# Kernel optimization log

Measured on AMD Instinct MI355X. Metric: run time of the kernel, lower is better.

The kernel has to match this reference:

```python
import jax, jax.numpy as jnp
import numpy as np

B, L, D, H, NL, F = 64, 197, 768, 12, 12, 3072
HD = D // H
EPS = 1e-6


def setup_inputs() -> dict:
    key = jax.random.key(0)
    ks = jax.random.split(key, 8)
    s = 0.02  # init std, matches nn.Parameter normal_(std=0.02) / xavier-ish scale
    def n(k, shape, scale=s):
        return jax.random.normal(k, shape, jnp.float32) * scale
    return {
        "x": jax.random.normal(ks[0], (B, L, D), jnp.float32),
        "pos_emb": n(ks[1], (1, L, D)),
        "ln1_g": jnp.ones((NL, D), jnp.float32),
        "ln1_b": jnp.zeros((NL, D), jnp.float32),
        "Wq": n(ks[2], (NL, D, D)), "bq": jnp.zeros((NL, D), jnp.float32),
        "Wk": n(ks[3], (NL, D, D)), "bk": jnp.zeros((NL, D), jnp.float32),
        "Wv": n(ks[4], (NL, D, D)), "bv": jnp.zeros((NL, D), jnp.float32),
        "Wo": n(ks[5], (NL, D, D)), "bo": jnp.zeros((NL, D), jnp.float32),
        "ln2_g": jnp.ones((NL, D), jnp.float32),
        "ln2_b": jnp.zeros((NL, D), jnp.float32),
        "W1": n(ks[6], (NL, D, F)), "b1": jnp.zeros((NL, F), jnp.float32),
        "W2": n(ks[7], (NL, F, D)), "b2": jnp.zeros((NL, D), jnp.float32),
        "lnf_g": jnp.ones((D,), jnp.float32),
        "lnf_b": jnp.zeros((D,), jnp.float32),
    }


def _ln(x, g, b):
    m = jnp.mean(x, axis=-1, keepdims=True)
    v = jnp.var(x, axis=-1, keepdims=True)
    return (x - m) * jax.lax.rsqrt(v + EPS) * g + b


def reference(x, pos_emb, ln1_g, ln1_b, Wq, bq, Wk, bk, Wv, bv, Wo, bo,
              ln2_g, ln2_b, W1, b1, W2, b2, lnf_g, lnf_b):
    Bv, Lv, Dv = x.shape
    nh = H
    hd = Dv // nh
    scale = 1.0 / np.sqrt(hd).astype(np.float32)

    def block(h, p):
        g1, be1, wq, bq_, wk, bk_, wv, bv_, wo, bo_, g2, be2, w1, bb1, w2, bb2 = p
        y = _ln(h, g1, be1)
        q = (y @ wq + bq_).reshape(Bv, Lv, nh, hd)
        k = (y @ wk + bk_).reshape(Bv, Lv, nh, hd)
        v = (y @ wv + bv_).reshape(Bv, Lv, nh, hd)
        scores = jnp.einsum('bqhd,bkhd->bhqk', q, k) * scale  # [B,H,L,L]
        a = jax.nn.softmax(scores, axis=-1)
        o = jnp.einsum('bhqk,bkhd->bqhd', a, v).reshape(Bv, Lv, Dv)
        h = h + (o @ wo + bo_)
        y = _ln(h, g2, be2)
        y = jax.nn.gelu(y @ w1 + bb1, approximate=False)
        y = y @ w2 + bb2
        return h + y, None

    params = (ln1_g, ln1_b, Wq, bq, Wk, bk, Wv, bv, Wo, bo,
              ln2_g, ln2_b, W1, b1, W2, b2)
    h = x + pos_emb
    h, _ = jax.lax.scan(block, h, params)
    return _ln(h, lnf_g, lnf_b)
```

## Files before the change

kernel.cpp:

```cpp
#include <hip/hip_runtime.h>
#include <hip/hip_bf16.h>
#include <cmath>

#define B_ 64
#define L_ 197
#define D_ 768
#define H_ 12
#define NL_ 12
#define F_ 3072
#define M_ (B_*L_)
#define MPAD_ 12672

typedef __bf16 bf16_t;
typedef __bf16 bf16x8 __attribute__((ext_vector_type(8)));
typedef __bf16 bf16x4 __attribute__((ext_vector_type(4)));
typedef float  f32x4  __attribute__((ext_vector_type(4)));

#define GPTR(p) ((const __attribute__((address_space(1))) void*)(p))
#define LPTR(p) ((__attribute__((address_space(3))) void*)(p))

__device__ __forceinline__ float gelu_f(float x) {
    return 0.5f * x * (1.f + erff(x * 0.70710678118654752440f));
}

__global__ __launch_bounds__(256) void k_addpos(const float4* __restrict__ x,
                                                const float4* __restrict__ pos,
                                                bf16x4* __restrict__ h,
                                                int n4, int ld4) {
    int i = blockIdx.x * 256 + threadIdx.x;
    if (i < n4) {
        float4 a = x[i];
        float4 p = pos[i % ld4];
        bf16x4 o;
        o[0] = (bf16_t)(a.x + p.x); o[1] = (bf16_t)(a.y + p.y);
        o[2] = (bf16_t)(a.z + p.z); o[3] = (bf16_t)(a.w + p.w);
        h[i] = o;
    }
}

__global__ __launch_bounds__(256) void k_prep(
        const float* __restrict__ Wq, const float* __restrict__ Wk,
        const float* __restrict__ Wv, const float* __restrict__ Wo,
        const float* __restrict__ W1, const float* __restrict__ W2,
        const float* __restrict__ bq, const float* __restrict__ bk,
        const float* __restrict__ bv,
        bf16_t* __restrict__ wqkvT, bf16_t* __restrict__ woT,
        bf16_t* __restrict__ w1T, bf16_t* __restrict__ w2T,
        float* __restrict__ bqkv) {
    int bidx = blockIdx.x;
    if (bidx < 3) {
        int i = bidx * 256 + threadIdx.x;
        if (i < D_) { bqkv[i] = bq[i]; bqkv[D_ + i] = bk[i]; bqkv[2*D_ + i] = bv[i]; }
        return;
    }
    int t = bidx - 3;
    const float* W; bf16_t* BT; int K, N;
    if (t < 576) {
        int seg = t / 144; t -= seg * 144;
        K = D_; N = D_;
        W  = (seg == 0 ? Wq : seg == 1 ? Wk : seg == 2 ? Wv : Wo);
        BT = (seg == 3 ? woT : wqkvT + (size_t)seg * 768 * D_);
    } else if (t < 1152) { t -= 576;  W = W1; BT = w1T; K = D_; N = F_; }
    else                 { t -= 1152; W = W2; BT = w2T; K = F_; N = D_; }
    const int kt = K / 64;
    const int k0 = (t % kt) * 64, n0 = (t / kt) * 64;

    __shared__ bf16_t s[64][67];
    int tid = threadIdx.x;
    int kr = tid >> 4, nc = (tid & 15) * 4;
    #pragma unroll
    for (int i = 0; i < 4; ++i) {
        float4 v = *(const float4*)(W + (size_t)(k0 + kr + i*16) * N + n0 + nc);
        s[kr + i*16][nc]     = (bf16_t)v.x;
        s[kr + i*16][nc + 1] = (bf16_t)v.y;
        s[kr + i*16][nc + 2] = (bf16_t)v.z;
        s[kr + i*16][nc + 3] = (bf16_t)v.w;
    }
    __syncthreads();
    int nr = tid >> 3, kc = (tid & 7) * 8;
    #pragma unroll
    for (int i = 0; i < 2; ++i) {
        bf16x8 o;
        #pragma unroll
        for (int j = 0; j < 8; ++j) o[j] = s[kc + j][nr + i*32];
        *(bf16x8*)(BT + (size_t)(n0 + nr + i*32) * K + k0 + kc) = o;
    }
}

template<bool BF16OUT>
__global__ __launch_bounds__(256) void k_ln(const bf16_t* __restrict__ x,
                                            const float* __restrict__ g,
                                            const float* __restrict__ bsh,
                                            void* __restrict__ out) {
    int wid = threadIdx.x >> 6, lane = threadIdx.x & 63;
    size_t row = (size_t)blockIdx.x * 4 + wid;
    const bf16x4* xr = (const bf16x4*)(x + row * D_);
    float vv[12];
    float s = 0.f, sq = 0.f;
    #pragma unroll
    for (int i = 0; i < 3; ++i) {
        bf16x4 v4 = xr[i*64 + lane];
        #pragma unroll
        for (int j = 0; j < 4; ++j) {
            float f = (float)v4[j];
            vv[i*4 + j] = f; s += f; sq += f*f;
        }
    }
    #pragma unroll
    for (int o = 1; o < 64; o <<= 1) { s += __shfl_xor(s, o); sq += __shfl_xor(sq, o); }
    float mean = s * (1.f/768.f);
    float var  = sq * (1.f/768.f) - mean*mean;
    float rstd = rsqrtf(var + 1e-6f);
    const float4* g4 = (const float4*)g;
    const float4* b4 = (const float4*)bsh;
    #pragma unroll
    for (int i = 0; i < 3; ++i) {
        float4 gg = g4[i*64 + lane], bb = b4[i*64 + lane];
        float r0 = (vv[i*4+0] - mean)*rstd*gg.x + bb.x;
        float r1 = (vv[i*4+1] - mean)*rstd*gg.y + bb.y;
        float r2 = (vv[i*4+2] - mean)*rstd*gg.z + bb.z;
        float r3 = (vv[i*4+3] - mean)*rstd*gg.w + bb.w;
        if (BF16OUT) {
            bf16x4 o4; o4[0]=(bf16_t)r0; o4[1]=(bf16_t)r1; o4[2]=(bf16_t)r2; o4[3]=(bf16_t)r3;
            ((bf16x4*)((bf16_t*)out + row * D_))[i*64 + lane] = o4;
        } else {
            float4 r; r.x=r0; r.y=r1; r.z=r2; r.w=r3;
            ((float4*)out)[row * (D_/4) + i*64 + lane] = r;
        }
    }
}

template<int EPI>
__global__ __launch_bounds__(256, 4) void k_gemm_bt(
        const bf16_t* __restrict__ A, const bf16_t* __restrict__ BT,
        const float* __restrict__ bias, const bf16_t* __restrict__ resid,
        void* __restrict__ Cout, int K, int N, int NB) {
    __shared__ bf16_t LDS_[2][128 * 64];
    bf16_t* As = LDS_[0];
    bf16_t* Bs = LDS_[1];

    const int tid = threadIdx.x, lane = tid & 63, wid = tid >> 6;
    const int g = lane >> 4, fr = lane & 15;
    const int wm = (wid >> 1) * 64, wn = (wid & 1) * 64;

    int nwg = (int)gridDim.x, orig = (int)blockIdx.x;
    int qq = nwg >> 3, rr = nwg & 7;
    int xcd = orig & 7, idx = orig >> 3;
    int wg = (xcd < rr ? xcd * (qq + 1) : rr * (qq + 1) + (xcd - rr) * qq) + idx;
    int bx = wg / NB, by = wg - bx * NB;
    const int gm0 = bx * 128, gn0 = by * 128;

    const int srl = lane >> 3;
    const int sc = ((lane & 7) ^ srl) * 8;

    f32x4 acc[4][4];
    #pragma unroll
    for (int i = 0; i < 4; ++i)
        #pragma unroll
        for (int j = 0; j < 4; ++j) acc[i][j] = (f32x4){0.f, 0.f, 0.f, 0.f};

    const bf16_t* a_src = A  + (size_t)(gm0 + wid * 32 + srl) * K + sc;
    const bf16_t* b_src = BT + (size_t)(gn0 + wid * 32 + srl) * K + sc;

    const int NT = K >> 6;
    for (int t = 0; t < NT; ++t) {
        const int k0 = t * 64;
        __syncthreads();
        #pragma unroll
        for (int i = 0; i < 4; ++i) {
            __builtin_amdgcn_global_load_lds(GPTR(a_src + (size_t)(i * 8) * K + k0),
                                             LPTR(&As[(wid * 32 + i * 8) * 64]), 16, 0, 0);
            __builtin_amdgcn_global_load_lds(GPTR(b_src + (size_t)(i * 8) * K + k0),
                                             LPTR(&Bs[(wid * 32 + i * 8) * 64]), 16, 0, 0);
        }
        __syncthreads();

        bf16x8 af[4][2], bf[4][2];
        #pragma unroll
        for (int mi = 0; mi < 4; ++mi) {
            const int row = wm + mi * 16 + fr;
            #pragma unroll
            for (int kc = 0; kc < 2; ++kc)
                af[mi][kc] = *(const bf16x8*)&As[row * 64 + (((kc * 4 + g) ^ (row & 7)) * 8)];
        }
        #pragma unroll
        for (int ni = 0; ni < 4; ++ni) {
            const int row = wn + ni * 16 + fr;
            #pragma unroll
            for (int kc = 0; kc < 2; ++kc)
                bf[ni][kc] = *(const bf16x8*)&Bs[row * 64 + (((kc * 4 + g) ^ (row & 7)) * 8)];
        }
        #pragma unroll
        for (int kc = 0; kc < 2; ++kc)
            #pragma unroll
            for (int mi = 0; mi < 4; ++mi)
                #pragma unroll
                for (int ni = 0; ni < 4; ++ni)
                    acc[mi][ni] = __builtin_amdgcn_mfma_f32_16x16x32_bf16(
                        af[mi][kc], bf[ni][kc], acc[mi][ni], 0, 0, 0);
    }

    if (EPI == 2) {
        float* Cf = (float*)&LDS_[0][0];
        #pragma unroll
        for (int h = 0; h < 2; ++h) {
            __syncthreads();
            if ((wid >> 1) == h) {
                #pragma unroll
                for (int mi = 0; mi < 4; ++mi)
                    #pragma unroll
                    for (int ni = 0; ni < 4; ++ni) {
                        const int c = wn + ni * 16 + fr;
                        const float bval = bias[gn0 + c];
                        #pragma unroll
                        for (int v = 0; v < 4; ++v) {
                            const int rl = mi * 16 + g * 4 + v;
                            Cf[rl * 128 + (((c >> 2) ^ (rl & 7)) << 2) + (c & 3)] =
                                acc[mi][ni][v] + bval;
                        }
                    }
            }
            __syncthreads();
            #pragma unroll
            for (int pass = 0; pass < 4; ++pass) {
                const int rl = pass * 16 + (tid >> 4);
                const int lc0 = (tid & 15) * 2;
                const int s2 = rl & 7;
                f32x4 lo = *(const f32x4*)&Cf[rl * 128 + ((lc0 ^ s2) << 2)];
                f32x4 hi = *(const f32x4*)&Cf[rl * 128 + (((lc0 + 1) ^ s2) << 2)];
                const int grow = gm0 + h * 64 + rl;
                if (grow < M_) {
                    const size_t base = (size_t)grow * N + gn0 + (tid & 15) * 8;
                    bf16x8 res = *(const bf16x8*)(resid + base);
                    bf16x8 o;
                    o[0] = (bf16_t)(lo[0] + (float)res[0]);
                    o[1] = (bf16_t)(lo[1] + (float)res[1]);
                    o[2] = (bf16_t)(lo[2] + (float)res[2]);
                    o[3] = (bf16_t)(lo[3] + (float)res[3]);
                    o[4] = (bf16_t)(hi[0] + (float)res[4]);
                    o[5] = (bf16_t)(hi[1] + (float)res[5]);
                    o[6] = (bf16_t)(hi[2] + (float)res[6]);
                    o[7] = (bf16_t)(hi[3] + (float)res[7]);
                    *(bf16x8*)((bf16_t*)Cout + base) = o;
                }
            }
        }
    } else {
        __syncthreads();
        bf16_t* Cs = &LDS_[0][0];
        #pragma unroll
        for (int mi = 0; mi < 4; ++mi)
            #pragma unroll
            for (int ni = 0; ni < 4; ++ni) {
                const int col = wn + ni * 16 + fr;
                const float bval = bias[gn0 + col];
                const int ch = col >> 3, co = col & 7;
                #pragma unroll
                for (int v = 0; v < 4; ++v) {
                    const int row = wm + mi * 16 + g * 4 + v;
                    float val = acc[mi][ni][v] + bval;
                    if (EPI == 1) val = gelu_f(val);
                    Cs[row * 128 + ((ch ^ (row & 7)) << 3) + co] = (bf16_t)val;
                }
            }
        __syncthreads();
        #pragma unroll
        for (int p = 0; p < 8; ++p) {
            const int row = p * 16 + (tid >> 4);
            const int ch  = tid & 15;
            const int grow = gm0 + row;
            bf16x8 cv = *(const bf16x8*)&Cs[row * 128 + ((ch ^ (row & 7)) << 3)];
            if (grow < M_)
                *(bf16x8*)((bf16_t*)Cout + (size_t)grow * N + gn0 + ch * 8) = cv;
        }
    }
}

__global__ __launch_bounds__(256) void k_attn(const bf16_t* __restrict__ qkv,
                                              bf16_t* __restrict__ out) {
    __shared__ bf16_t VT[64][232];
    __shared__ bf16_t P[4][16][232];
    int tid = threadIdx.x, lane = tid & 63, wid = tid >> 6;
    int b = blockIdx.x / H_, hh = blockIdx.x % H_;
    const size_t base = (size_t)b * L_ * 2304 + hh * 64;

    for (int r = tid >> 3; r < L_; r += 32) {
        int cg = (tid & 7) * 8;
        bf16x8 vv = *(const bf16x8*)(qkv + base + (size_t)r * 2304 + 1536 + cg);
        #pragma unroll
        for (int j = 0; j < 8; ++j) VT[cg + j][r] = vv[j];
    }
    for (int i = tid; i < 64 * 35; i += 256) VT[i / 35][197 + i % 35] = (bf16_t)0.f;
    {
        int r = lane & 15, c0 = 208 + (lane >> 4) * 4;
        #pragma unroll
        for (int j = 0; j < 4; ++j) P[wid][r][c0 + j] = (bf16_t)0.f;
    }
    __syncthreads();

    for (int s = wid; s < 13; s += 4) {
        int q0 = s * 16;
        int qr = q0 + (lane & 15); if (qr > L_ - 1) qr = L_ - 1;
        bf16x8 qf[2];
        #pragma unroll
        for (int kk = 0; kk < 2; ++kk)
            qf[kk] = *(const bf16x8*)(qkv + base + (size_t)qr * 2304 + kk * 32 + (lane >> 4) * 8);

        f32x4 sacc[13];
        #pragma unroll
        for (int nb = 0; nb < 13; ++nb) { f32x4 z = {0.f,0.f,0.f,0.f}; sacc[nb] = z; }
        #pragma unroll
        for (int nb = 0; nb < 13; ++nb) {
            int lk = nb * 16 + (lane & 15); if (lk > L_ - 1) lk = L_ - 1;
            #pragma unroll
            for (int kk = 0; kk < 2; ++kk) {
                bf16x8 kf = *(const bf16x8*)(qkv + base + (size_t)lk * 2304 + D_ + kk * 32 + (lane >> 4) * 8);
                sacc[nb] = __builtin_amdgcn_mfma_f32_16x16x32_bf16(qf[kk], kf, sacc[nb], 0, 0, 0);
            }
        }

        float mx[4] = {-1e30f, -1e30f, -1e30f, -1e30f};
        float pv[13][4];
        #pragma unroll
        for (int nb = 0; nb < 13; ++nb) {
            bool valid = (nb * 16 + (lane & 15)) < L_;
            #pragma unroll
            for (int v = 0; v < 4; ++v) {
                float sv = valid ? sacc[nb][v] * 0.125f : -1e30f;
                pv[nb][v] = sv;
                mx[v] = fmaxf(mx[v], sv);
            }
        }
        #pragma unroll
        for (int o = 1; o < 16; o <<= 1) {
            #pragma unroll
            for (int v = 0; v < 4; ++v) mx[v] = fmaxf(mx[v], __shfl_xor(mx[v], o));
        }
        float sum[4] = {0.f, 0.f, 0.f, 0.f};
        #pragma unroll
        for (int nb = 0; nb < 13; ++nb) {
            bool valid = (nb * 16 + (lane & 15)) < L_;
            #pragma unroll
            for (int v = 0; v < 4; ++v) {
                float e2 = valid ? __expf(pv[nb][v] - mx[v]) : 0.f;
                pv[nb][v] = e2; sum[v] += e2;
            }
        }
        #pragma unroll
        for (int o = 1; o < 16; o <<= 1) {
            #pragma unroll
            for (int v = 0; v < 4; ++v) sum[v] += __shfl_xor(sum[v], o);
        }

        #pragma unroll
        for (int nb = 0; nb < 13; ++nb)
            #pragma unroll
            for (int v = 0; v < 4; ++v)
                P[wid][(lane >> 4) * 4 + v][nb * 16 + (lane & 15)] = (bf16_t)pv[nb][v];
        asm volatile("s_waitcnt lgkmcnt(0)" ::: "memory");

        f32x4 oacc[4];
        #pragma unroll
        for (int nb = 0; nb < 4; ++nb) { f32x4 z = {0.f,0.f,0.f,0.f}; oacc[nb] = z; }
        #pragma unroll
        for (int kk = 0; kk < 7; ++kk) {
            bf16x8 pf = *(const bf16x8*)&P[wid][lane & 15][kk * 32 + (lane >> 4) * 8];
            #pragma unroll
            for (int nb = 0; nb < 4; ++nb) {
                bf16x8 vf = *(const bf16x8*)&VT[nb * 16 + (lane & 15)][kk * 32 + (lane >> 4) * 8];
                oacc[nb] = __builtin_amdgcn_mfma_f32_16x16x32_bf16(pf, vf, oacc[nb], 0, 0, 0);
            }
        }

        float rs[4];
        #pragma unroll
        for (int v = 0; v < 4; ++v) rs[v] = 1.f / sum[v];
        #pragma unroll
        for (int nb = 0; nb < 4; ++nb)
            #pragma unroll
            for (int v = 0; v < 4; ++v) {
                int r = q0 + (lane >> 4) * 4 + v;
                if (r < L_)
                    out[((size_t)b * L_ + r) * D_ + hh * 64 + nb * 16 + (lane & 15)] =
                        (bf16_t)(oacc[nb][v] * rs[v]);
            }
    }
}

extern "C" void kernel_launch(void* const* d_in, const int* in_sizes, int n_in,
                              void* d_out, int out_size, void* d_ws, size_t ws_size,
                              hipStream_t stream) {
    const float* x     = (const float*)d_in[0];
    const float* pos   = (const float*)d_in[1];
    const float* ln1_g = (const float*)d_in[2];
    const float* ln1_b = (const float*)d_in[3];
    const float* Wq    = (const float*)d_in[4];
    const float* bq    = (const float*)d_in[5];
    const float* Wk    = (const float*)d_in[6];
    const float* bk    = (const float*)d_in[7];
    const float* Wv    = (const float*)d_in[8];
    const float* bv    = (const float*)d_in[9];
    const float* Wo    = (const float*)d_in[10];
    const float* bo    = (const float*)d_in[11];
    const float* ln2_g = (const float*)d_in[12];
    const float* ln2_b = (const float*)d_in[13];
    const float* W1    = (const float*)d_in[14];
    const float* b1    = (const float*)d_in[15];
    const float* W2    = (const float*)d_in[16];
    const float* b2    = (const float*)d_in[17];
    const float* lnf_g = (const float*)d_in[18];
    const float* lnf_b = (const float*)d_in[19];

    char* wsp = (char*)d_ws;
    size_t off = 0;
    auto alloc = [&](size_t bytes) -> void* {
        void* r = wsp + off;
        off += (bytes + 255) & ~(size_t)255;
        return r;
    };
    bf16_t* h     = (bf16_t*)alloc((size_t)M_ * D_ * 2);
    bf16_t* y     = (bf16_t*)alloc((size_t)MPAD_ * D_ * 2);
    bf16_t* qkv   = (bf16_t*)alloc((size_t)M_ * 2304 * 2);
    bf16_t* attn  = (bf16_t*)alloc((size_t)MPAD_ * D_ * 2);
    bf16_t* u     = (bf16_t*)alloc((size_t)MPAD_ * F_ * 2);
    bf16_t* wqkvT = (bf16_t*)alloc((size_t)2304 * D_ * 2);
    bf16_t* woT   = (bf16_t*)alloc((size_t)D_ * D_ * 2);
    bf16_t* w1T   = (bf16_t*)alloc((size_t)F_ * D_ * 2);
    bf16_t* w2T   = (bf16_t*)alloc((size_t)D_ * F_ * 2);
    float*  bqkv  = (float*) alloc(2304 * 4);
    (void)ws_size; (void)in_sizes; (void)n_in; (void)out_size;

    {
        int n4 = M_ * D_ / 4;
        k_addpos<<<(n4 + 255) / 256, 256, 0, stream>>>((const float4*)x, (const float4*)pos,
                                                       (bf16x4*)h, n4, L_ * D_ / 4);
    }

    for (int l = 0; l < NL_; ++l) {
        k_prep<<<1731, 256, 0, stream>>>(Wq + (size_t)l * D_ * D_, Wk + (size_t)l * D_ * D_,
                                         Wv + (size_t)l * D_ * D_, Wo + (size_t)l * D_ * D_,
                                         W1 + (size_t)l * D_ * F_, W2 + (size_t)l * F_ * D_,
                                         bq + l * D_, bk + l * D_, bv + l * D_,
                                         wqkvT, woT, w1T, w2T, bqkv);

        k_ln<true><<<M_ / 4, 256, 0, stream>>>(h, ln1_g + l * D_, ln1_b + l * D_, y);
        k_gemm_bt<0><<<dim3(99 * 18), 256, 0, stream>>>(y,    wqkvT, bqkv,                nullptr, qkv, D_, 2304, 18);
        k_attn<<<B_ * H_, 256, 0, stream>>>(qkv, attn);
        k_gemm_bt<2><<<dim3(99 * 6),  256, 0, stream>>>(attn, woT,   bo + l * D_,         h,       h,   D_, D_,   6);
        k_ln<true><<<M_ / 4, 256, 0, stream>>>(h, ln2_g + l * D_, ln2_b + l * D_, y);
        k_gemm_bt<1><<<dim3(99 * 24), 256, 0, stream>>>(y,    w1T,   b1 + (size_t)l * F_, nullptr, u,   D_, F_,   24);
        k_gemm_bt<2><<<dim3(99 * 6),  256, 0, stream>>>(u,    w2T,   b2 + l * D_,         h,       h,   F_, D_,   6);
    }
    k_ln<false><<<M_ / 4, 256, 0, stream>>>(h, lnf_g, lnf_b, d_out);
}
```

Measured before the change: 3.694 ms.

## Fuse next-layer weight prep into FFN1 GEMM grid with double-buffered weights

Weight conversion and transposition for layer l+1 now runs as extra workgroups appended to layer l's FFN1 GEMM launch, using ping-pong weight buffers. Only layer 0 keeps a standalone prep launch. This removes the serialized prep kernel from each layer and lets it fill idle CUs during the GEMM tail. The cost is extra workspace, and the GEMM kernel signature now takes an explicit workgroup count used for the XCD remapping.

```diff
diff --git a/kernel.cpp b/kernel.cpp
--- a/kernel.cpp
+++ b/kernel.cpp
@@ -10,6 +10,7 @@
 #define F_ 3072
 #define M_ (B_*L_)
 #define MPAD_ 12672
+#define NPREP_ 1731
 
 typedef __bf16 bf16_t;
 typedef __bf16 bf16x8 __attribute__((ext_vector_type(8)));
@@ -21,6 +22,53 @@
 
 __device__ __forceinline__ float gelu_f(float x) {
     return 0.5f * x * (1.f + erff(x * 0.70710678118654752440f));
+}
+
+struct PrepArgs {
+    const float *Wq, *Wk, *Wv, *Wo, *W1, *W2, *bq, *bk, *bv;
+    bf16_t *wqkvT, *woT, *w1T, *w2T;
+    float *bqkv;
+};
+
+__device__ __forceinline__ void prep_body(int bidx, int tid, const PrepArgs& pa, void* lds) {
+    if (bidx < 3) {
+        int i = bidx * 256 + tid;
+        if (i < D_) {
+            pa.bqkv[i] = pa.bq[i]; pa.bqkv[D_ + i] = pa.bk[i]; pa.bqkv[2*D_ + i] = pa.bv[i];
+        }
+        return;
+    }
+    int t = bidx - 3;
+    const float* W; bf16_t* BT; int K, N;
+    if (t < 576) {
+        int seg = t / 144; t -= seg * 144;
+        K = D_; N = D_;
+        W  = (seg == 0 ? pa.Wq : seg == 1 ? pa.Wk : seg == 2 ? pa.Wv : pa.Wo);
+        BT = (seg == 3 ? pa.woT : pa.wqkvT + (size_t)seg * 768 * D_);
+    } else if (t < 1152) { t -= 576;  W = pa.W1; BT = pa.w1T; K = D_; N = F_; }
+    else                 { t -= 1152; W = pa.W2; BT = pa.w2T; K = F_; N = D_; }
+    const int kt = K / 64;
+    const int k0 = (t % kt) * 64, n0 = (t / kt) * 64;
+
+    bf16_t (*s)[67] = (bf16_t(*)[67])lds;
+    int kr = tid >> 4, nc = (tid & 15) * 4;
+    #pragma unroll
+    for (int i = 0; i < 4; ++i) {
+        float4 v = *(const float4*)(W + (size_t)(k0 + kr + i*16) * N + n0 + nc);
+        s[kr + i*16][nc]     = (bf16_t)v.x;
+        s[kr + i*16][nc + 1] = (bf16_t)v.y;
+        s[kr + i*16][nc + 2] = (bf16_t)v.z;
+        s[kr + i*16][nc + 3] = (bf16_t)v.w;
+    }
+    __syncthreads();
+    int nr = tid >> 3, kc = (tid & 7) * 8;
+    #pragma unroll
+    for (int i = 0; i < 2; ++i) {
+        bf16x8 o;
+        #pragma unroll
+        for (int j = 0; j < 8; ++j) o[j] = s[kc + j][nr + i*32];
+        *(bf16x8*)(BT + (size_t)(n0 + nr + i*32) * K + k0 + kc) = o;
+    }
 }
 
 __global__ __launch_bounds__(256) void k_addpos(const float4* __restrict__ x,
@@ -38,53 +86,9 @@
     }
 }
 
-__global__ __launch_bounds__(256) void k_prep(
-        const float* __restrict__ Wq, const float* __restrict__ Wk,
-        const float* __restrict__ Wv, const float* __restrict__ Wo,
-        const float* __restrict__ W1, const float* __restrict__ W2,
-        const float* __restrict__ bq, const float* __restrict__ bk,
-        const float* __restrict__ bv,
-        bf16_t* __restrict__ wqkvT, bf16_t* __restrict__ woT,
-        bf16_t* __restrict__ w1T, bf16_t* __restrict__ w2T,
-        float* __restrict__ bqkv) {
-    int bidx = blockIdx.x;
-    if (bidx < 3) {
-        int i = bidx * 256 + threadIdx.x;
-        if (i < D_) { bqkv[i] = bq[i]; bqkv[D_ + i] = bk[i]; bqkv[2*D_ + i] = bv[i]; }
-        return;
-    }
-    int t = bidx - 3;
-    const float* W; bf16_t* BT; int K, N;
-    if (t < 576) {
-        int seg = t / 144; t -= seg * 144;
-        K = D_; N = D_;
-        W  = (seg == 0 ? Wq : seg == 1 ? Wk : seg == 2 ? Wv : Wo);
-        BT = (seg == 3 ? woT : wqkvT + (size_t)seg * 768 * D_);
-    } else if (t < 1152) { t -= 576;  W = W1; BT = w1T; K = D_; N = F_; }
-    else                 { t -= 1152; W = W2; BT = w2T; K = F_; N = D_; }
-    const int kt = K / 64;
-    const int k0 = (t % kt) * 64, n0 = (t / kt) * 64;
-
+__global__ __launch_bounds__(256) void k_prep(PrepArgs pa) {
     __shared__ bf16_t s[64][67];
-    int tid = threadIdx.x;
-    int kr = tid >> 4, nc = (tid & 15) * 4;
-    #pragma unroll
-    for (int i = 0; i < 4; ++i) {
-        float4 v = *(const float4*)(W + (size_t)(k0 + kr + i*16) * N + n0 + nc);
-        s[kr + i*16][nc]     = (bf16_t)v.x;
-        s[kr + i*16][nc + 1] = (bf16_t)v.y;
-        s[kr + i*16][nc + 2] = (bf16_t)v.z;
-        s[kr + i*16][nc + 3] = (bf16_t)v.w;
-    }
-    __syncthreads();
-    int nr = tid >> 3, kc = (tid & 7) * 8;
-    #pragma unroll
-    for (int i = 0; i < 2; ++i) {
-        bf16x8 o;
-        #pragma unroll
-        for (int j = 0; j < 8; ++j) o[j] = s[kc + j][nr + i*32];
-        *(bf16x8*)(BT + (size_t)(n0 + nr + i*32) * K + k0 + kc) = o;
-    }
+    prep_body(blockIdx.x, threadIdx.x, pa, (void*)s);
 }
 
 template<bool BF16OUT>
@@ -130,20 +134,26 @@
     }
 }
 
-template<int EPI>
+template<int EPI, bool PREP>
 __global__ __launch_bounds__(256, 4) void k_gemm_bt(
         const bf16_t* __restrict__ A, const bf16_t* __restrict__ BT,
         const float* __restrict__ bias, const bf16_t* __restrict__ resid,
-        void* __restrict__ Cout, int K, int N, int NB) {
+        void* __restrict__ Cout, int K, int N, int NB, int nwg, PrepArgs pa) {
     __shared__ bf16_t LDS_[2][128 * 64];
     bf16_t* As = LDS_[0];
     bf16_t* Bs = LDS_[1];
 
     const int tid = threadIdx.x, lane = tid & 63, wid = tid >> 6;
+
+    if (PREP && (int)blockIdx.x >= nwg) {
+        prep_body((int)blockIdx.x - nwg, tid, pa, (void*)LDS_);
+        return;
+    }
+
     const int g = lane >> 4, fr = lane & 15;
     const int wm = (wid >> 1) * 64, wn = (wid & 1) * 64;
 
-    int nwg = (int)gridDim.x, orig = (int)blockIdx.x;
+    int orig = (int)blockIdx.x;
     int qq = nwg >> 3, rr = nwg & 7;
     int xcd = orig & 7, idx = orig >> 3;
     int wg = (xcd < rr ? xcd * (qq + 1) : rr * (qq + 1) + (xcd - rr) * qq) + idx;
@@ -423,33 +433,54 @@
     bf16_t* qkv   = (bf16_t*)alloc((size_t)M_ * 2304 * 2);
     bf16_t* attn  = (bf16_t*)alloc((size_t)MPAD_ * D_ * 2);
     bf16_t* u     = (bf16_t*)alloc((size_t)MPAD_ * F_ * 2);
-    bf16_t* wqkvT = (bf16_t*)alloc((size_t)2304 * D_ * 2);
-    bf16_t* woT   = (bf16_t*)alloc((size_t)D_ * D_ * 2);
-    bf16_t* w1T   = (bf16_t*)alloc((size_t)F_ * D_ * 2);
-    bf16_t* w2T   = (bf16_t*)alloc((size_t)D_ * F_ * 2);
-    float*  bqkv  = (float*) alloc(2304 * 4);
+    bf16_t* wqkvT[2]; bf16_t* woT[2]; bf16_t* w1T[2]; bf16_t* w2T[2]; float* bqkv[2];
+    for (int p = 0; p < 2; ++p) {
+        wqkvT[p] = (bf16_t*)alloc((size_t)2304 * D_ * 2);
+        woT[p]   = (bf16_t*)alloc((size_t)D_ * D_ * 2);
+        w1T[p]   = (bf16_t*)alloc((size_t)F_ * D_ * 2);
+        w2T[p]   = (bf16_t*)alloc((size_t)D_ * F_ * 2);
+        bqkv[p]  = (float*) alloc(2304 * 4);
+    }
     (void)ws_size; (void)in_sizes; (void)n_in; (void)out_size;
+
+    auto mkprep = [&](int l) -> PrepArgs {
+        int p = l & 1;
+        PrepArgs pa;
+        pa.Wq = Wq + (size_t)l * D_ * D_; pa.Wk = Wk + (size_t)l * D_ * D_;
+        pa.Wv = Wv + (size_t)l * D_ * D_; pa.Wo = Wo + (size_t)l * D_ * D_;
+        pa.W1 = W1 + (size_t)l * D_ * F_; pa.W2 = W2 + (size_t)l * F_ * D_;
+        pa.bq = bq + l * D_; pa.bk = bk + l * D_; pa.bv = bv + l * D_;
+        pa.wqkvT = wqkvT[p]; pa.woT = woT[p]; pa.w1T = w1T[p]; pa.w2T = w2T[p];
+        pa.bqkv = bqkv[p];
+        return pa;
+    };
+    PrepArgs nopa = {};
 
     {
         int n4 = M_ * D_ / 4;
         k_addpos<<<(n4 + 255) / 256, 256, 0, stream>>>((const float4*)x, (const float4*)pos,
                                                        (bf16x4*)h, n4, L_ * D_ / 4);
     }
+    k_prep<<<NPREP_, 256, 0, stream>>>(mkprep(0));
 
     for (int l = 0; l < NL_; ++l) {
-        k_prep<<<1731, 256, 0, stream>>>(Wq + (size_t)l * D_ * D_, Wk + (size_t)l * D_ * D_,
-                                         Wv + (size_t)l * D_ * D_, Wo + (size_t)l * D_ * D_,
-                                         W1 + (size_t)l * D_ * F_, W2 + (size_t)l * F_ * D_,
-                                         bq + l * D_, bk + l * D_, bv + l * D_,
-                                         wqkvT, woT, w1T, w2T, bqkv);
-
+        const int p = l & 1;
         k_ln<true><<<M_ / 4, 256, 0, stream>>>(h, ln1_g + l * D_, ln1_b + l * D_, y);
-        k_gemm_bt<0><<<dim3(99 * 18), 256, 0, stream>>>(y,    wqkvT, bqkv,                nullptr, qkv, D_, 2304, 18);
+        k_gemm_bt<0, false><<<dim3(99 * 18), 256, 0, stream>>>(
+            y, wqkvT[p], bqkv[p], nullptr, qkv, D_, 2304, 18, 99 * 18, nopa);
         k_attn<<<B_ * H_, 256, 0, stream>>>(qkv, attn);
-        k_gemm_bt<2><<<dim3(99 * 6),  256, 0, stream>>>(attn, woT,   bo + l * D_,         h,       h,   D_, D_,   6);
+        k_gemm_bt<2, false><<<dim3(99 * 6), 256, 0, stream>>>(
+            attn, woT[p], bo + l * D_, h, h, D_, D_, 6, 99 * 6, nopa);
         k_ln<true><<<M_ / 4, 256, 0, stream>>>(h, ln2_g + l * D_, ln2_b + l * D_, y);
-        k_gemm_bt<1><<<dim3(99 * 24), 256, 0, stream>>>(y,    w1T,   b1 + (size_t)l * F_, nullptr, u,   D_, F_,   24);
-        k_gemm_bt<2><<<dim3(99 * 6),  256, 0, stream>>>(u,    w2T,   b2 + l * D_,         h,       h,   F_, D_,   6);
+        if (l + 1 < NL_) {
+            k_gemm_bt<1, true><<<dim3(99 * 24 + NPREP_), 256, 0, stream>>>(
+                y, w1T[p], b1 + (size_t)l * F_, nullptr, u, D_, F_, 24, 99 * 24, mkprep(l + 1));
+        } else {
+            k_gemm_bt<1, false><<<dim3(99 * 24), 256, 0, stream>>>(
+                y, w1T[p], b1 + (size_t)l * F_, nullptr, u, D_, F_, 24, 99 * 24, nopa);
+        }
+        k_gemm_bt<2, false><<<dim3(99 * 6), 256, 0, stream>>>(
+            u, w2T[p], b2 + l * D_, h, h, F_, D_, 6, 99 * 6, nopa);
     }
     k_ln<false><<<M_ / 4, 256, 0, stream>>>(h, lnf_g, lnf_b, d_out);
 }
```

New measurement: 3.592 ms (median of 2 runs). 2.8% less time.
